# Performance work log

Measured on AMD Instinct MI355X. Metric: run time of the kernel, lower is better.

The kernel has to match this reference:

```python
import jax, jax.numpy as jnp
import numpy as np


def setup_inputs() -> dict:
    key = jax.random.key(0)
    k1, k2 = jax.random.split(key)
    B, D1, D2 = 32768, 1024, 4096
    g1 = jax.random.normal(k1, (B, D1), dtype=jnp.float32)
    # Learned parameter, initialized as in the module: N(0,1)*0.02 + 0.2
    W = jax.random.normal(k2, (D1, D2), dtype=jnp.float32) * 0.02 + 0.2
    return {"g1": g1, "W": W}


def reference(g1, W):
    beta = 10.0
    # Column-normalize W: each column divided by its L2 norm. [d1, d2]
    nc = jnp.sqrt(jnp.sum(W ** 2, axis=0, keepdims=True))
    nW = W / nc
    # Similarity scores. [B, d2]
    x2 = g1 @ nW
    # Scaled logsumexp energy. [B]
    return -1.0 / beta * jax.nn.logsumexp(beta * x2, axis=-1)
```

## Files before the change

### kernel.cpp

```cpp
#include <hip/hip_runtime.h>
#include <hip/hip_bf16.h>
#include <hip/hip_fp8.h>

typedef int i32x8 __attribute__((ext_vector_type(8)));
typedef int i32x4 __attribute__((ext_vector_type(4)));
typedef float f32x4 __attribute__((ext_vector_type(4)));
typedef unsigned char uchar_t;

constexpr int NB = 32768;
constexpr int D1 = 1024;
constexpr int D2 = 4096;
constexpr float BETA_LOG2E = 14.4269504088896340736f;
constexpr float SCALE_A = 16.0f;
constexpr float SCALE_B = 8192.0f;
constexpr float INV_SCALE = 1.0f / (16.0f * 8192.0f);

__device__ __forceinline__ uchar_t f32_to_fp8(float f) {
  __hip_fp8_e4m3 q(f);
  return (uchar_t)q.__x;
}

__device__ __forceinline__ void async_copy16(const void* g, void* l) {
  __builtin_amdgcn_global_load_lds(
      (const __attribute__((address_space(1))) void*)g,
      (__attribute__((address_space(3))) void*)l, 16, 0, 0);
}

__global__ void colstats(const float* __restrict__ W, float* __restrict__ sq,
                         float* __restrict__ colsum) {
  int j = blockIdx.x * 256 + threadIdx.x;
  int k0 = blockIdx.y * 64;
  float a = 0.f, b = 0.f;
#pragma unroll 8
  for (int k = 0; k < 64; ++k) {
    float w = W[(size_t)(k0 + k) * D2 + j];
    a += w * w; b += w;
  }
  atomicAdd(&sq[j], a);
  atomicAdd(&colsum[j], b);
}

__global__ void convert_a(const float* __restrict__ g1, uchar_t* __restrict__ A8,
                          float* __restrict__ S) {
  int row = blockIdx.x;
  int t = threadIdx.x;
  const float* src = g1 + (size_t)row * D1 + t * 8;
  float v[8];
  *(float4*)(v)     = *(const float4*)(src);
  *(float4*)(v + 4) = *(const float4*)(src + 4);
  float sum = 0.f;
  union { uchar_t b[8]; uint2 u; } o;
#pragma unroll
  for (int j = 0; j < 8; ++j) { sum += v[j]; o.b[j] = f32_to_fp8(v[j] * SCALE_A); }
  *(uint2*)(A8 + (size_t)row * D1 + t * 8) = o.u;
#pragma unroll
  for (int m = 1; m < 64; m <<= 1) sum += __shfl_xor(sum, m, 64);
  __shared__ float part[2];
  if ((t & 63) == 0) part[t >> 6] = sum;
  __syncthreads();
  if (t == 0) S[row] = part[0] + part[1];
}

__global__ void convert_b(const float* __restrict__ W, const float* __restrict__ sq,
                          const float* __restrict__ colsum,
                          uchar_t* __restrict__ B8t, float* __restrict__ mu) {
  __shared__ float tile[64][65];
  int t = threadIdx.x;
  int j0 = blockIdx.x * 64;
  int k0 = blockIdx.y * 64;
  int c = t & 63, r4 = t >> 6;
#pragma unroll
  for (int s = 0; s < 16; ++s) {
    int k = s * 4 + r4;
    tile[k][c] = W[(size_t)(k0 + k) * D2 + j0 + c];
  }
  __syncthreads();
#pragma unroll
  for (int s = 0; s < 16; ++s) {
    int jj = s * 4 + r4;
    float inv = 1.0f / sqrtf(sq[j0 + jj]);
    float muj = colsum[j0 + jj] * inv * (1.0f / 1024.0f);
    if (k0 == 0 && c == 0) mu[j0 + jj] = muj;
    float dw = tile[c][jj] * inv - muj;
    B8t[(size_t)(j0 + jj) * D1 + k0 + c] = f32_to_fp8(dw * SCALE_B);
  }
}

__global__ __launch_bounds__(256, 2)
void gemm_expsum(const uchar_t* __restrict__ A8, const uchar_t* __restrict__ B8t,
                 const float* __restrict__ S, const float* __restrict__ mu,
                 float* __restrict__ s) {
  __shared__ __align__(16) uchar_t As[2 * 128 * 128];
  __shared__ __align__(16) uchar_t Bs[2 * 128 * 128];

  const int t = threadIdx.x;
  const int row0 = blockIdx.y * 128;
  const int col0 = blockIdx.x * 128;
  const int lane = t & 63;
  const int wave = t >> 6;
  const int wm = (wave >> 1) * 64;
  const int wn = (wave & 1) * 64;
  const int llo = lane & 15, lhi = lane >> 4;

  f32x4 acc[4][4] = {};

  const int srow = t >> 3;
  const int sseg = (t & 7) ^ (srow & 7);
  const uchar_t* gA = A8  + (size_t)(row0 + srow) * D1 + sseg * 16;
  const uchar_t* gB = B8t + (size_t)(col0 + srow) * D1 + sseg * 16;

  const int sw0 = ((lhi * 2 + 0) ^ (llo & 7)) * 16;
  const int sw1 = ((lhi * 2 + 1) ^ (llo & 7)) * 16;

#pragma unroll
  for (int i = 0; i < 4; ++i) {
    async_copy16(gA + (size_t)i * 32 * D1, As + t * 16 + i * 4096);
    async_copy16(gB + (size_t)i * 32 * D1, Bs + t * 16 + i * 4096);
  }

  int p = 0;
  for (int kt = 0; kt < D1; kt += 128, p ^= 1) {
    __syncthreads();
    if (kt + 128 < D1) {
#pragma unroll
      for (int i = 0; i < 4; ++i) {
        async_copy16(gA + (size_t)i * 32 * D1 + kt + 128,
                     As + (p ^ 1) * 16384 + t * 16 + i * 4096);
        async_copy16(gB + (size_t)i * 32 * D1 + kt + 128,
                     Bs + (p ^ 1) * 16384 + t * 16 + i * 4096);
      }
    }
    const uchar_t* baseA = As + p * 16384;
    const uchar_t* baseB = Bs + p * 16384;
    i32x8 af[4], bq[4];
#pragma unroll
    for (int mi = 0; mi < 4; ++mi) {
      const uchar_t* q = baseA + (wm + mi * 16 + llo) * 128;
      i32x4 h0 = *(const i32x4*)(q + sw0);
      i32x4 h1 = *(const i32x4*)(q + sw1);
      af[mi] = __builtin_shufflevector(h0, h1, 0, 1, 2, 3, 4, 5, 6, 7);
    }
#pragma unroll
    for (int ni = 0; ni < 4; ++ni) {
      const uchar_t* q = baseB + (wn + ni * 16 + llo) * 128;
      i32x4 h0 = *(const i32x4*)(q + sw0);
      i32x4 h1 = *(const i32x4*)(q + sw1);
      bq[ni] = __builtin_shufflevector(h0, h1, 0, 1, 2, 3, 4, 5, 6, 7);
    }
#pragma unroll
    for (int mi = 0; mi < 4; ++mi)
#pragma unroll
      for (int ni = 0; ni < 4; ++ni)
        acc[mi][ni] = __builtin_amdgcn_mfma_scale_f32_16x16x128_f8f6f4(
            af[mi], bq[ni], acc[mi][ni],
            0, 0,
            0, 127,
            0, 127);
  }

  float muv[4];
#pragma unroll
  for (int ni = 0; ni < 4; ++ni) muv[ni] = mu[col0 + wn + ni * 16 + llo];

#pragma unroll
  for (int mi = 0; mi < 4; ++mi) {
    const int row = row0 + wm + mi * 16 + lhi * 4;
    float4 sv = *(const float4*)(S + row);
    float sarr[4] = {sv.x, sv.y, sv.z, sv.w};
    float rs[4];
#pragma unroll
    for (int r = 0; r < 4; ++r) {
      float v = 0.f;
#pragma unroll
      for (int ni = 0; ni < 4; ++ni) {
        float x2 = fmaf(acc[mi][ni][r], INV_SCALE, muv[ni] * sarr[r]);
        v += exp2f(x2 * BETA_LOG2E);
      }
      rs[r] = v;
    }
#pragma unroll
    for (int m = 1; m < 16; m <<= 1) {
#pragma unroll
      for (int r = 0; r < 4; ++r)
        rs[r] += __shfl_xor(rs[r], m, 64);
    }
    if (llo == 0) {
#pragma unroll
      for (int r = 0; r < 4; ++r)
        atomicAdd(&s[row + r], rs[r]);
    }
  }
}

__global__ void finish_kernel(const float* __restrict__ s, float* __restrict__ out) {
  int b = blockIdx.x * 256 + threadIdx.x;
  out[b] = -0.1f * logf(s[b]);
}

extern "C" void kernel_launch(void* const* d_in, const int* in_sizes, int n_in,
                              void* d_out, int out_size, void* d_ws, size_t ws_size,
                              hipStream_t stream) {
  const float* g1 = (const float*)d_in[0];
  const float* W  = (const float*)d_in[1];
  float* out = (float*)d_out;

  char* ws = (char*)d_ws;
  float* s       = (float*)ws;
  float* sq      = (float*)(ws + 131072);
  float* colsum  = (float*)(ws + 147456);
  float* mu      = (float*)(ws + 163840);
  float* S       = (float*)(ws + 180224);
  uchar_t* A8    = (uchar_t*)(ws + 311296);
  uchar_t* B8t   = (uchar_t*)(ws + 311296 + 33554432);

  hipMemsetAsync(ws, 0, 180224, stream);

  colstats<<<dim3(16, 16), 256, 0, stream>>>(W, sq, colsum);
  convert_b<<<dim3(64, 16), 256, 0, stream>>>(W, sq, colsum, B8t, mu);
  convert_a<<<dim3(32768), 128, 0, stream>>>(g1, A8, S);
  gemm_expsum<<<dim3(32, 256), 256, 0, stream>>>(A8, B8t, S, mu, s);
  finish_kernel<<<dim3(128), 256, 0, stream>>>(s, out);
}
```

Measured before the change: 421.0 us.

## Enlarge GEMM tiles to 256x256 with staged prefetch, fuse W prep, grid-stride A conversion

The fp8 GEMM moves from 128x128 tiles with 4 waves to 256x256 tiles with 8 waves. Each wave now computes 128x64, and the k-loop is split into three phases that interleave async LDS loads of the next tile with MFMA work, using explicit vmcnt waits, barriers and setprio. The aim is to raise arithmetic intensity and hide global-load latency. Column statistics and W conversion are fused into one kernel, which removes the atomics, a memset region and a launch, and convert_a becomes a grid-stride kernel with 16 elements per lane. The risks are that prep_b runs on only 64 blocks, and that the larger tile and accumulator footprint (32 accumulators per lane, 128KB LDS) may reduce occupancy.

New measurement: 907.9 us. +115.7%, slower.

```diff
diff --git a/kernel.cpp b/kernel.cpp
--- a/kernel.cpp
+++ b/kernel.cpp
@@ -26,168 +26,220 @@
       (__attribute__((address_space(3))) void*)l, 16, 0, 0);
 }
 
-__global__ void colstats(const float* __restrict__ W, float* __restrict__ sq,
-                         float* __restrict__ colsum) {
-  int j = blockIdx.x * 256 + threadIdx.x;
-  int k0 = blockIdx.y * 64;
+__global__ __launch_bounds__(256)
+void prep_b(const float* __restrict__ W, uchar_t* __restrict__ B8t,
+            float* __restrict__ mu) {
+  __shared__ float sqs[4][64], css[4][64];
+  __shared__ float sinv[64], smu[64];
+  __shared__ float tile[64][65];
+  const int t = threadIdx.x;
+  const int j0 = blockIdx.x * 64;
+  const int c = t & 63, g = t >> 6;
   float a = 0.f, b = 0.f;
+  const float* wp = W + (size_t)(g * 256) * D2 + j0 + c;
 #pragma unroll 8
-  for (int k = 0; k < 64; ++k) {
-    float w = W[(size_t)(k0 + k) * D2 + j];
-    a += w * w; b += w;
-  }
-  atomicAdd(&sq[j], a);
-  atomicAdd(&colsum[j], b);
-}
-
-__global__ void convert_a(const float* __restrict__ g1, uchar_t* __restrict__ A8,
-                          float* __restrict__ S) {
-  int row = blockIdx.x;
-  int t = threadIdx.x;
-  const float* src = g1 + (size_t)row * D1 + t * 8;
-  float v[8];
-  *(float4*)(v)     = *(const float4*)(src);
-  *(float4*)(v + 4) = *(const float4*)(src + 4);
-  float sum = 0.f;
-  union { uchar_t b[8]; uint2 u; } o;
-#pragma unroll
-  for (int j = 0; j < 8; ++j) { sum += v[j]; o.b[j] = f32_to_fp8(v[j] * SCALE_A); }
-  *(uint2*)(A8 + (size_t)row * D1 + t * 8) = o.u;
-#pragma unroll
-  for (int m = 1; m < 64; m <<= 1) sum += __shfl_xor(sum, m, 64);
-  __shared__ float part[2];
-  if ((t & 63) == 0) part[t >> 6] = sum;
+  for (int k = 0; k < 256; ++k) { float w = wp[(size_t)k * D2]; a += w * w; b += w; }
+  sqs[g][c] = a; css[g][c] = b;
   __syncthreads();
-  if (t == 0) S[row] = part[0] + part[1];
-}
-
-__global__ void convert_b(const float* __restrict__ W, const float* __restrict__ sq,
-                          const float* __restrict__ colsum,
-                          uchar_t* __restrict__ B8t, float* __restrict__ mu) {
-  __shared__ float tile[64][65];
-  int t = threadIdx.x;
-  int j0 = blockIdx.x * 64;
-  int k0 = blockIdx.y * 64;
-  int c = t & 63, r4 = t >> 6;
-#pragma unroll
-  for (int s = 0; s < 16; ++s) {
-    int k = s * 4 + r4;
-    tile[k][c] = W[(size_t)(k0 + k) * D2 + j0 + c];
+  if (t < 64) {
+    float sq = sqs[0][t] + sqs[1][t] + sqs[2][t] + sqs[3][t];
+    float cs = css[0][t] + css[1][t] + css[2][t] + css[3][t];
+    float inv = 1.0f / sqrtf(sq);
+    float m = cs * inv * (1.0f / 1024.0f);
+    sinv[t] = inv; smu[t] = m; mu[j0 + t] = m;
   }
   __syncthreads();
-#pragma unroll
-  for (int s = 0; s < 16; ++s) {
-    int jj = s * 4 + r4;
-    float inv = 1.0f / sqrtf(sq[j0 + jj]);
-    float muj = colsum[j0 + jj] * inv * (1.0f / 1024.0f);
-    if (k0 == 0 && c == 0) mu[j0 + jj] = muj;
-    float dw = tile[c][jj] * inv - muj;
-    B8t[(size_t)(j0 + jj) * D1 + k0 + c] = f32_to_fp8(dw * SCALE_B);
-  }
-}
-
-__global__ __launch_bounds__(256, 2)
+  const int r4 = t >> 6;
+  for (int k0 = 0; k0 < 1024; k0 += 64) {
+#pragma unroll
+    for (int s = 0; s < 16; ++s) {
+      int k = s * 4 + r4;
+      tile[k][c] = W[(size_t)(k0 + k) * D2 + j0 + c];
+    }
+    __syncthreads();
+#pragma unroll
+    for (int s = 0; s < 16; ++s) {
+      int jj = s * 4 + r4;
+      float dw = tile[c][jj] * sinv[jj] - smu[jj];
+      B8t[(size_t)(j0 + jj) * D1 + k0 + c] = f32_to_fp8(dw * SCALE_B);
+    }
+    __syncthreads();
+  }
+}
+
+__global__ __launch_bounds__(256)
+void convert_a(const float* __restrict__ g1, uchar_t* __restrict__ A8,
+               float* __restrict__ S) {
+  const int lane = threadIdx.x & 63;
+  const int gw = (blockIdx.x * 256 + threadIdx.x) >> 6;
+  for (int row = gw; row < NB; row += 8192) {
+    const float* src = g1 + (size_t)row * D1 + lane * 16;
+    float v[16];
+    *(float4*)(v)      = ((const float4*)src)[0];
+    *(float4*)(v + 4)  = ((const float4*)src)[1];
+    *(float4*)(v + 8)  = ((const float4*)src)[2];
+    *(float4*)(v + 12) = ((const float4*)src)[3];
+    float sum = 0.f;
+    union { uchar_t b[16]; uint4 u; } o;
+#pragma unroll
+    for (int j = 0; j < 16; ++j) { sum += v[j]; o.b[j] = f32_to_fp8(v[j] * SCALE_A); }
+    *(uint4*)(A8 + (size_t)row * D1 + lane * 16) = o.u;
+#pragma unroll
+    for (int m = 1; m < 64; m <<= 1) sum += __shfl_xor(sum, m, 64);
+    if (lane == 0) S[row] = sum;
+  }
+}
+
+__global__ __launch_bounds__(512, 2)
 void gemm_expsum(const uchar_t* __restrict__ A8, const uchar_t* __restrict__ B8t,
                  const float* __restrict__ S, const float* __restrict__ mu,
                  float* __restrict__ s) {
-  __shared__ __align__(16) uchar_t As[2 * 128 * 128];
-  __shared__ __align__(16) uchar_t Bs[2 * 128 * 128];
+  __shared__ __align__(16) uchar_t As[2 * 256 * 128];
+  __shared__ __align__(16) uchar_t Bs[2 * 256 * 128];
 
   const int t = threadIdx.x;
-  const int row0 = blockIdx.y * 128;
-  const int col0 = blockIdx.x * 128;
+  const int row0 = blockIdx.y * 256;
+  const int col0 = blockIdx.x * 256;
   const int lane = t & 63;
   const int wave = t >> 6;
-  const int wm = (wave >> 1) * 64;
-  const int wn = (wave & 1) * 64;
+  const int wm = (wave >> 2) * 128;
+  const int wn = (wave & 3) * 64;
   const int llo = lane & 15, lhi = lane >> 4;
 
-  f32x4 acc[4][4] = {};
-
-  const int srow = t >> 3;
-  const int sseg = (t & 7) ^ (srow & 7);
-  const uchar_t* gA = A8  + (size_t)(row0 + srow) * D1 + sseg * 16;
-  const uchar_t* gB = B8t + (size_t)(col0 + srow) * D1 + sseg * 16;
+  f32x4 acc[8][4] = {};
+
+  const int r   = t >> 3;
+  const int rB  = ((r >> 5) << 6) + (r & 31);
+  const int seg = t & 7;
+  const int swz = seg ^ (r & 7);
+  const uchar_t* gA = A8  + (size_t)(row0 + r ) * D1 + swz * 16;
+  const uchar_t* gB = B8t + (size_t)(col0 + rB) * D1 + swz * 16;
+  uchar_t* lA = As + r  * 128 + seg * 16;
+  uchar_t* lB = Bs + rB * 128 + seg * 16;
+
+#define ISSUE_A0(kt, bo) { async_copy16(gA + (kt),              lA + (bo)); \
+                           async_copy16(gA + (kt) + 128 * 1024, lA + (bo) + 128 * 128); }
+#define ISSUE_B0(kt, bo) { async_copy16(gB + (kt),              lB + (bo)); \
+                           async_copy16(gB + (kt) + 128 * 1024, lB + (bo) + 128 * 128); }
+#define ISSUE_B1(kt, bo) { async_copy16(gB + (kt) +  32 * 1024, lB + (bo) +  32 * 128); \
+                           async_copy16(gB + (kt) + 160 * 1024, lB + (bo) + 160 * 128); }
+#define ISSUE_A1(kt, bo) { async_copy16(gA + (kt) +  64 * 1024, lA + (bo) +  64 * 128); \
+                           async_copy16(gA + (kt) + 192 * 1024, lA + (bo) + 192 * 128); }
 
   const int sw0 = ((lhi * 2 + 0) ^ (llo & 7)) * 16;
   const int sw1 = ((lhi * 2 + 1) ^ (llo & 7)) * 16;
 
-#pragma unroll
-  for (int i = 0; i < 4; ++i) {
-    async_copy16(gA + (size_t)i * 32 * D1, As + t * 16 + i * 4096);
-    async_copy16(gB + (size_t)i * 32 * D1, Bs + t * 16 + i * 4096);
-  }
-
-  int p = 0;
-  for (int kt = 0; kt < D1; kt += 128, p ^= 1) {
-    __syncthreads();
-    if (kt + 128 < D1) {
-#pragma unroll
-      for (int i = 0; i < 4; ++i) {
-        async_copy16(gA + (size_t)i * 32 * D1 + kt + 128,
-                     As + (p ^ 1) * 16384 + t * 16 + i * 4096);
-        async_copy16(gB + (size_t)i * 32 * D1 + kt + 128,
-                     Bs + (p ^ 1) * 16384 + t * 16 + i * 4096);
-      }
-    }
-    const uchar_t* baseA = As + p * 16384;
-    const uchar_t* baseB = Bs + p * 16384;
+  ISSUE_A0(0, 0); ISSUE_B0(0, 0); ISSUE_B1(0, 0); ISSUE_A1(0, 0);
+  asm volatile("s_waitcnt vmcnt(4)" ::: "memory");
+  __builtin_amdgcn_s_barrier();
+
+  for (int T = 0; T < 8; ++T) {
+    const int p = T & 1;
+    const int kt1 = ((T + 1) & 7) * 128;
+    const int bo1 = (p ^ 1) * 32768;
+    const uchar_t* baseA = As + p * 32768;
+    const uchar_t* baseB = Bs + p * 32768;
     i32x8 af[4], bq[4];
-#pragma unroll
-    for (int mi = 0; mi < 4; ++mi) {
-      const uchar_t* q = baseA + (wm + mi * 16 + llo) * 128;
-      i32x4 h0 = *(const i32x4*)(q + sw0);
-      i32x4 h1 = *(const i32x4*)(q + sw1);
-      af[mi] = __builtin_shufflevector(h0, h1, 0, 1, 2, 3, 4, 5, 6, 7);
-    }
-#pragma unroll
-    for (int ni = 0; ni < 4; ++ni) {
-      const uchar_t* q = baseB + (wn + ni * 16 + llo) * 128;
-      i32x4 h0 = *(const i32x4*)(q + sw0);
-      i32x4 h1 = *(const i32x4*)(q + sw1);
-      bq[ni] = __builtin_shufflevector(h0, h1, 0, 1, 2, 3, 4, 5, 6, 7);
-    }
-#pragma unroll
-    for (int mi = 0; mi < 4; ++mi)
-#pragma unroll
-      for (int ni = 0; ni < 4; ++ni)
-        acc[mi][ni] = __builtin_amdgcn_mfma_scale_f32_16x16x128_f8f6f4(
-            af[mi], bq[ni], acc[mi][ni],
-            0, 0,
-            0, 127,
-            0, 127);
-  }
+
+    ISSUE_A0(kt1, bo1); ISSUE_B0(kt1, bo1);
+#pragma unroll
+    for (int q = 0; q < 4; ++q) {
+      const uchar_t* a = baseA + (wm + q * 16 + llo) * 128;
+      i32x4 h0 = *(const i32x4*)(a + sw0);
+      i32x4 h1 = *(const i32x4*)(a + sw1);
+      af[q] = __builtin_shufflevector(h0, h1, 0, 1, 2, 3, 4, 5, 6, 7);
+    }
+#pragma unroll
+    for (int j = 0; j < 2; ++j) {
+      const uchar_t* b = baseB + (wn + j * 16 + llo) * 128;
+      i32x4 h0 = *(const i32x4*)(b + sw0);
+      i32x4 h1 = *(const i32x4*)(b + sw1);
+      bq[j] = __builtin_shufflevector(h0, h1, 0, 1, 2, 3, 4, 5, 6, 7);
+    }
+    __builtin_amdgcn_s_setprio(1);
+#pragma unroll
+    for (int q = 0; q < 4; ++q)
+#pragma unroll
+      for (int j = 0; j < 2; ++j)
+        acc[q][j] = __builtin_amdgcn_mfma_scale_f32_16x16x128_f8f6f4(
+            af[q], bq[j], acc[q][j], 0, 0, 0, 127, 0, 127);
+    __builtin_amdgcn_s_setprio(0);
+    asm volatile("s_waitcnt vmcnt(6)" ::: "memory");
+    __builtin_amdgcn_s_barrier();
+
+    ISSUE_B1(kt1, bo1);
+#pragma unroll
+    for (int j = 0; j < 2; ++j) {
+      const uchar_t* b = baseB + (wn + (2 + j) * 16 + llo) * 128;
+      i32x4 h0 = *(const i32x4*)(b + sw0);
+      i32x4 h1 = *(const i32x4*)(b + sw1);
+      bq[2 + j] = __builtin_shufflevector(h0, h1, 0, 1, 2, 3, 4, 5, 6, 7);
+    }
+    __builtin_amdgcn_s_setprio(1);
+#pragma unroll
+    for (int q = 0; q < 4; ++q)
+#pragma unroll
+      for (int j = 0; j < 2; ++j)
+        acc[q][2 + j] = __builtin_amdgcn_mfma_scale_f32_16x16x128_f8f6f4(
+            af[q], bq[2 + j], acc[q][2 + j], 0, 0, 0, 127, 0, 127);
+    __builtin_amdgcn_s_setprio(0);
+    asm volatile("s_waitcnt vmcnt(6)" ::: "memory");
+    __builtin_amdgcn_s_barrier();
+
+    ISSUE_A1(kt1, bo1);
+#pragma unroll
+    for (int q = 0; q < 4; ++q) {
+      const uchar_t* a = baseA + (wm + 64 + q * 16 + llo) * 128;
+      i32x4 h0 = *(const i32x4*)(a + sw0);
+      i32x4 h1 = *(const i32x4*)(a + sw1);
+      af[q] = __builtin_shufflevector(h0, h1, 0, 1, 2, 3, 4, 5, 6, 7);
+    }
+    __builtin_amdgcn_s_setprio(1);
+#pragma unroll
+    for (int q = 0; q < 4; ++q)
+#pragma unroll
+      for (int j = 0; j < 4; ++j)
+        acc[4 + q][j] = __builtin_amdgcn_mfma_scale_f32_16x16x128_f8f6f4(
+            af[q], bq[j], acc[4 + q][j], 0, 0, 0, 127, 0, 127);
+    __builtin_amdgcn_s_setprio(0);
+    asm volatile("s_waitcnt vmcnt(4)" ::: "memory");
+    __builtin_amdgcn_s_barrier();
+  }
+#undef ISSUE_A0
+#undef ISSUE_B0
+#undef ISSUE_B1
+#undef ISSUE_A1
 
   float muv[4];
 #pragma unroll
   for (int ni = 0; ni < 4; ++ni) muv[ni] = mu[col0 + wn + ni * 16 + llo];
 
 #pragma unroll
-  for (int mi = 0; mi < 4; ++mi) {
+  for (int mi = 0; mi < 8; ++mi) {
     const int row = row0 + wm + mi * 16 + lhi * 4;
     float4 sv = *(const float4*)(S + row);
     float sarr[4] = {sv.x, sv.y, sv.z, sv.w};
     float rs[4];
 #pragma unroll
-    for (int r = 0; r < 4; ++r) {
+    for (int rr = 0; rr < 4; ++rr) {
       float v = 0.f;
 #pragma unroll
       for (int ni = 0; ni < 4; ++ni) {
-        float x2 = fmaf(acc[mi][ni][r], INV_SCALE, muv[ni] * sarr[r]);
+        float x2 = fmaf(acc[mi][ni][rr], INV_SCALE, muv[ni] * sarr[rr]);
         v += exp2f(x2 * BETA_LOG2E);
       }
-      rs[r] = v;
+      rs[rr] = v;
     }
 #pragma unroll
     for (int m = 1; m < 16; m <<= 1) {
 #pragma unroll
-      for (int r = 0; r < 4; ++r)
-        rs[r] += __shfl_xor(rs[r], m, 64);
+      for (int rr = 0; rr < 4; ++rr)
+        rs[rr] += __shfl_xor(rs[rr], m, 64);
     }
     if (llo == 0) {
 #pragma unroll
-      for (int r = 0; r < 4; ++r)
-        atomicAdd(&s[row + r], rs[r]);
+      for (int rr = 0; rr < 4; ++rr)
+        atomicAdd(&s[row + rr], rs[rr]);
     }
   }
 }
@@ -206,18 +258,15 @@
 
   char* ws = (char*)d_ws;
   float* s       = (float*)ws;
-  float* sq      = (float*)(ws + 131072);
-  float* colsum  = (float*)(ws + 147456);
-  float* mu      = (float*)(ws + 163840);
-  float* S       = (float*)(ws + 180224);
-  uchar_t* A8    = (uchar_t*)(ws + 311296);
-  uchar_t* B8t   = (uchar_t*)(ws + 311296 + 33554432);
-
-  hipMemsetAsync(ws, 0, 180224, stream);
-
-  colstats<<<dim3(16, 16), 256, 0, stream>>>(W, sq, colsum);
-  convert_b<<<dim3(64, 16), 256, 0, stream>>>(W, sq, colsum, B8t, mu);
-  convert_a<<<dim3(32768), 128, 0, stream>>>(g1, A8, S);
-  gemm_expsum<<<dim3(32, 256), 256, 0, stream>>>(A8, B8t, S, mu, s);
+  float* mu      = (float*)(ws + 131072);
+  float* S       = (float*)(ws + 147456);
+  uchar_t* A8    = (uchar_t*)(ws + 278528);
+  uchar_t* B8t   = (uchar_t*)(ws + 278528 + 33554432);
+
+  hipMemsetAsync(ws, 0, 131072, stream);
+
+  prep_b<<<dim3(64), 256, 0, stream>>>(W, B8t, mu);
+  convert_a<<<dim3(2048), 256, 0, stream>>>(g1, A8, S);
+  gemm_expsum<<<dim3(16, 128), 512, 0, stream>>>(A8, B8t, S, mu, s);
   finish_kernel<<<dim3(128), 256, 0, stream>>>(s, out);
 }
```
